# Performance work log

Measured on AMD Instinct MI355X. Metric: run time of the kernel, lower is better.

The kernel has to match this reference:

```python
import jax, jax.numpy as jnp
import numpy as np

N_NODES = 100000
N_EDGES = 1250000
IN_NDIM = 128
OUT_NDIM = 64


def setup_inputs() -> dict:
    key = jax.random.key(0)
    ks = jax.random.split(key, 8)
    return {
        "node_feats": jax.random.normal(ks[0], (N_NODES, IN_NDIM), dtype=jnp.float32),
        "edge_d": jax.random.uniform(ks[1], (N_EDGES, 1), dtype=jnp.float32),
        "W0": jax.random.normal(ks[2], (1, 1), dtype=jnp.float32),
        "W1": jax.random.normal(ks[3], (OUT_NDIM, IN_NDIM), dtype=jnp.float32) * (IN_NDIM ** -0.5),
        "W2": jax.random.normal(ks[4], (OUT_NDIM, IN_NDIM), dtype=jnp.float32) * (IN_NDIM ** -0.5),
        "Wa": jax.random.normal(ks[5], (1, 2 * OUT_NDIM + 1), dtype=jnp.float32) * (OUT_NDIM ** -0.5),
        "src": jax.random.randint(ks[6], (N_EDGES,), 0, N_NODES, dtype=jnp.int32),
        "dst": jax.random.randint(ks[7], (N_EDGES,), 0, N_NODES, dtype=jnp.int32),
    }


def reference(node_feats, edge_d, W0, W1, W2, Wa, src, dst):
    N = node_feats.shape[0]
    # fc1 / fc2 node projections (bias-free linears)
    z = node_feats @ W1.T            # [N, out_ndim]
    z_i = node_feats @ W2.T          # [N, out_ndim]
    # fc0 edge feature projection
    t = edge_d @ W0.T                # [E, 1]
    # gather per-edge endpoint features
    z_src = z[src]                   # [E, out_ndim]
    z_dst = z[dst]                   # [E, out_ndim]
    # attention logit: leaky_relu(attn_fc([z_src, z_dst, t]))
    a = jnp.concatenate([z_src, z_dst, t], axis=1) @ Wa.T   # [E, 1]
    e = jax.nn.leaky_relu(a[:, 0], 0.01)                      # torch default slope
    # segment softmax over incoming edges of each dst node
    m = jax.ops.segment_max(e, dst, num_segments=N)          # -inf for empty segs
    ex = jnp.exp(e - m[dst])
    denom = jax.ops.segment_sum(ex, dst, num_segments=N)
    alpha = ex / denom[dst]                                   # [E]
    # weighted scatter-sum of source messages
    z_neighbor = jax.ops.segment_sum(alpha[:, None] * z_src, dst, num_segments=N)
    h = jax.nn.relu(z_i + z_neighbor)
    return h
```

## Files before the change

kernel.cpp:

```cpp
#include <hip/hip_runtime.h>

#define N_NODES 100000
#define N_EDGES 1250000
#define IN_D 128
#define OUT_D 64
#define BSHIFT 8
#define NBUCK  391
#define CAP    4608
#define EPB    4096
#define NBLK_E 306
#define NBLK_G 1563

typedef __attribute__((ext_vector_type(8))) __bf16 bf16x8;
typedef __attribute__((ext_vector_type(4))) float floatx4;

__device__ __forceinline__ float2 up2(unsigned u) {
    return make_float2(__uint_as_float(u << 16),
                       __uint_as_float(u & 0xFFFF0000u));
}

__global__ __launch_bounds__(256) void fusedA_kernel(
    const float* __restrict__ x, const float* __restrict__ W1,
    const float* __restrict__ W2, const float* __restrict__ W0,
    const float* __restrict__ Wa,
    const int* __restrict__ dst, const int* __restrict__ src,
    const float* __restrict__ edge_d,
    int* __restrict__ gcur, uint2* __restrict__ payA,
    unsigned short* __restrict__ zb, unsigned short* __restrict__ zib,
    float* __restrict__ s1, float* __restrict__ s2)
{
    __shared__ __bf16 sB[16384];
    __shared__ float  sWa[128];
    __shared__ int    h[NBUCK];
    __shared__ int    lcur[NBUCK];

    const int t = threadIdx.x;

    if (blockIdx.x < NBLK_E) {
        const float tc = W0[0] * Wa[2 * OUT_D];
        for (int i = t; i < NBUCK; i += 256) h[i] = 0;
        __syncthreads();
        const int base = blockIdx.x * EPB;
        for (int k0 = 0; k0 < EPB; k0 += 1024) {
            int i = base + k0 + t * 4;
            if (i < N_EDGES) {
                int4 d4 = *(const int4*)(dst + i);
                atomicAdd(&h[d4.x >> BSHIFT], 1);
                atomicAdd(&h[d4.y >> BSHIFT], 1);
                atomicAdd(&h[d4.z >> BSHIFT], 1);
                atomicAdd(&h[d4.w >> BSHIFT], 1);
            }
        }
        __syncthreads();
        for (int b = t; b < NBUCK; b += 256) {
            int hc = h[b];
            int p = hc ? atomicAdd(&gcur[b], hc) : 0;
            lcur[b] = b * CAP + p;
        }
        __syncthreads();
        #define EMIT(dv, sv, ev)                                              \
            { int bk = (dv) >> BSHIFT;                                        \
              int pos = atomicAdd(&lcur[bk], 1);                              \
              if (pos < (bk + 1) * CAP)                                       \
                  payA[pos] = make_uint2((unsigned)(sv) |                     \
                                         ((unsigned)((dv) & 255) << 17),      \
                                         __float_as_uint(tc * (ev))); }
        for (int k0 = 0; k0 < EPB; k0 += 1024) {
            int i = base + k0 + t * 4;
            if (i < N_EDGES) {
                int4   d4 = *(const int4*)(dst + i);
                int4   s4 = *(const int4*)(src + i);
                float4 e4 = *(const float4*)(edge_d + i);
                EMIT(d4.x, s4.x, e4.x);
                EMIT(d4.y, s4.y, e4.y);
                EMIT(d4.z, s4.z, e4.z);
                EMIT(d4.w, s4.w, e4.w);
            }
        }
        #undef EMIT
        return;
    }

    #pragma unroll
    for (int g = 0; g < 8; ++g) {
        int gi = t + g * 256;
        int n  = gi >> 4;
        int k8 = gi & 15;
        const float* wrow = (n < 64) ? (W1 + n * 128) : (W2 + (n - 64) * 128);
        float4 v0 = *(const float4*)(wrow + k8 * 8);
        float4 v1 = *(const float4*)(wrow + k8 * 8 + 4);
        int lane = ((k8 & 3) << 4) | (n & 15);
        int off  = (((n >> 4) * 4 + (k8 >> 2)) * 64 + lane) * 8;
        bf16x8 bb;
        bb[0] = (__bf16)v0.x; bb[1] = (__bf16)v0.y;
        bb[2] = (__bf16)v0.z; bb[3] = (__bf16)v0.w;
        bb[4] = (__bf16)v1.x; bb[5] = (__bf16)v1.y;
        bb[6] = (__bf16)v1.z; bb[7] = (__bf16)v1.w;
        *(bf16x8*)(sB + off) = bb;
    }
    if (t < 128) sWa[t] = Wa[t];
    __syncthreads();

    const int lane = t & 63;
    const int wave = t >> 6;
    const int tile = (blockIdx.x - NBLK_E) * 4 + wave;
    if (tile * 16 >= N_NODES) return;

    const int n0 = tile * 16;
    const int m  = lane & 15;
    const int kb = lane >> 4;

    floatx4 acc[8];
    #pragma unroll
    for (int q = 0; q < 8; ++q) acc[q] = (floatx4)(0.f);

    const float* xrow = x + (size_t)(n0 + m) * IN_D;

    #pragma unroll
    for (int kc = 0; kc < 4; ++kc) {
        float4 v0 = *(const float4*)(xrow + kc * 32 + kb * 8);
        float4 v1 = *(const float4*)(xrow + kc * 32 + kb * 8 + 4);
        float xs[8] = {v0.x, v0.y, v0.z, v0.w, v1.x, v1.y, v1.z, v1.w};
        bf16x8 ahi, alo;
        #pragma unroll
        for (int j = 0; j < 8; ++j) {
            __bf16 hh = (__bf16)xs[j];
            ahi[j] = hh;
            alo[j] = (__bf16)(xs[j] - (float)hh);
        }
        #pragma unroll
        for (int nt = 0; nt < 8; ++nt) {
            int off = ((nt * 4 + kc) * 64 + lane) * 8;
            bf16x8 b = *(const bf16x8*)(sB + off);
            acc[nt] = __builtin_amdgcn_mfma_f32_16x16x32_bf16(ahi, b, acc[nt], 0, 0, 0);
            acc[nt] = __builtin_amdgcn_mfma_f32_16x16x32_bf16(alo, b, acc[nt], 0, 0, 0);
        }
    }

    #pragma unroll
    for (int nt = 0; nt < 8; ++nt) {
        int col = (nt & 3) * 16 + m;
        unsigned short* dp = (nt < 4) ? zb : zib;
        #pragma unroll
        for (int reg = 0; reg < 4; ++reg) {
            int row = n0 + kb * 4 + reg;
            __bf16 hh = (__bf16)acc[nt][reg];
            dp[(size_t)row * OUT_D + col] = *(unsigned short*)&hh;
        }
    }

    #pragma unroll
    for (int reg = 0; reg < 4; ++reg) {
        float p1 = 0.f, p2 = 0.f;
        #pragma unroll
        for (int nt = 0; nt < 4; ++nt) {
            float zv = acc[nt][reg];
            p1 += zv * sWa[nt * 16 + m];
            p2 += zv * sWa[64 + nt * 16 + m];
        }
        #pragma unroll
        for (int off = 8; off > 0; off >>= 1) {
            p1 += __shfl_xor(p1, off);
            p2 += __shfl_xor(p2, off);
        }
        if (m == 0) {
            int row = n0 + kb * 4 + reg;
            s1[row] = p1;
            s2[row] = p2;
        }
    }
}

__global__ __launch_bounds__(512) void passB_kernel(
    const int* __restrict__ gcur, const uint2* __restrict__ payA,
    int2* __restrict__ node_meta, uint2* __restrict__ payB)
{
    __shared__ int h[256];
    __shared__ int lc[256];
    __shared__ int sm[256];

    const int b = blockIdx.x, t = threadIdx.x;
    const int base = b * CAP;
    const int cnt = min(gcur[b], CAP);
    const int n0 = b << BSHIFT;

    if (t < 256) h[t] = 0;
    __syncthreads();

    for (int i0 = t * 4; i0 < cnt; i0 += 2048) {
        uint4 u0 = *(const uint4*)(payA + base + i0);
        uint4 u1 = *(const uint4*)(payA + base + i0 + 2);
        atomicAdd(&h[(u0.x >> 17) & 255], 1);
        if (i0 + 1 < cnt) atomicAdd(&h[(u0.z >> 17) & 255], 1);
        if (i0 + 2 < cnt) atomicAdd(&h[(u1.x >> 17) & 255], 1);
        if (i0 + 3 < cnt) atomicAdd(&h[(u1.z >> 17) & 255], 1);
    }
    __syncthreads();

    if (t < 256) {
        int v = h[t];
        sm[t] = v;
        __syncthreads();
        for (int off = 1; off < 256; off <<= 1) {
            int add = (t >= off) ? sm[t - off] : 0;
            __syncthreads();
            sm[t] += add;
            __syncthreads();
        }
        int start = base + sm[t] - v;
        lc[t] = start;
        if (n0 + t < N_NODES) node_meta[n0 + t] = make_int2(start, v);
    } else {
        __syncthreads();
        for (int off = 1; off < 256; off <<= 1) {
            __syncthreads(); __syncthreads();
        }
    }
    __syncthreads();

    #define PUT(xx, yy, ok)                                                   \
        if (ok) { int j = ((xx) >> 17) & 255;                                 \
                  int pos = atomicAdd(&lc[j], 1);                             \
                  payB[pos] = make_uint2((xx) & 0x1FFFFu, (yy)); }
    for (int i0 = t * 4; i0 < cnt; i0 += 2048) {
        uint4 u0 = *(const uint4*)(payA + base + i0);
        uint4 u1 = *(const uint4*)(payA + base + i0 + 2);
        PUT(u0.x, u0.y, true);
        PUT(u0.z, u0.w, i0 + 1 < cnt);
        PUT(u1.x, u1.y, i0 + 2 < cnt);
        PUT(u1.z, u1.w, i0 + 3 < cnt);
    }
    #undef PUT
}

__global__ __launch_bounds__(256) void gather_finalize_kernel(
    const int2* __restrict__ node_meta, const uint2* __restrict__ payB,
    const float* __restrict__ s1, const float* __restrict__ s2,
    const unsigned short* __restrict__ zb, const unsigned short* __restrict__ zib,
    float* __restrict__ out)
{
    __shared__ uint2 buf[8][32];

    const int lane = threadIdx.x & 63;
    const int wave = threadIdx.x >> 6;
    const int half = lane >> 5;
    const int lh   = lane & 31;
    const int nodeSlot = wave * 2 + half;
    const int d = blockIdx.x * 8 + nodeSlot;

    const int2 meta = node_meta[d];
    const int beg = meta.x;
    const int len = meta.y;
    const float s2d = s2[d];

    const int eC = lh >> 3;
    const int c  = lh & 7;

    float den = 0.f;
    float2 a0 = make_float2(0.f, 0.f), a1 = a0, a2 = a0, a3 = a0;

    for (int o = 0; o < len; o += 32) {
        int rem = len - o;
        bool v = lh < rem;
        uint2 p = payB[beg + o + (v ? lh : 0)];
        float ex = 0.f;
        if (v) {
            float a = __uint_as_float(p.y) + s1[p.x] + s2d;
            float e = (a > 0.f) ? a : 0.01f * a;
            ex = __expf(e);
            buf[nodeSlot][lh] = make_uint2(p.x, __float_as_uint(ex));
        }
        den += ex;

        int cnt = min(32, rem);
        for (int g = 0; g * 4 < cnt; ++g) {
            int j = g * 4 + eC;
            uint2 pe = buf[nodeSlot][(j < cnt) ? j : 0];
            float exe = (j < cnt) ? __uint_as_float(pe.y) : 0.f;
            uint4 zv = *(const uint4*)(zb + (size_t)pe.x * OUT_D + c * 8);
            float2 w0 = up2(zv.x), w1 = up2(zv.y), w2 = up2(zv.z), w3 = up2(zv.w);
            a0.x = fmaf(exe, w0.x, a0.x); a0.y = fmaf(exe, w0.y, a0.y);
            a1.x = fmaf(exe, w1.x, a1.x); a1.y = fmaf(exe, w1.y, a1.y);
            a2.x = fmaf(exe, w2.x, a2.x); a2.y = fmaf(exe, w2.y, a2.y);
            a3.x = fmaf(exe, w3.x, a3.x); a3.y = fmaf(exe, w3.y, a3.y);
        }
    }

    #pragma unroll
    for (int off = 16; off > 0; off >>= 1) den += __shfl_xor(den, off);
    #pragma unroll
    for (int off = 8; off <= 16; off <<= 1) {
        a0.x += __shfl_xor(a0.x, off); a0.y += __shfl_xor(a0.y, off);
        a1.x += __shfl_xor(a1.x, off); a1.y += __shfl_xor(a1.y, off);
        a2.x += __shfl_xor(a2.x, off); a2.y += __shfl_xor(a2.y, off);
        a3.x += __shfl_xor(a3.x, off); a3.y += __shfl_xor(a3.y, off);
    }

    if (lh < 8) {
        float inv = (den > 0.f) ? 1.f / den : 0.f;
        uint4 zv = *(const uint4*)(zib + (size_t)d * OUT_D + lh * 8);
        float2 w0 = up2(zv.x), w1 = up2(zv.y), w2 = up2(zv.z), w3 = up2(zv.w);
        float4 o0, o1;
        o0.x = fmaxf(w0.x + a0.x * inv, 0.f);
        o0.y = fmaxf(w0.y + a0.y * inv, 0.f);
        o0.z = fmaxf(w1.x + a1.x * inv, 0.f);
        o0.w = fmaxf(w1.y + a1.y * inv, 0.f);
        o1.x = fmaxf(w2.x + a2.x * inv, 0.f);
        o1.y = fmaxf(w2.y + a2.y * inv, 0.f);
        o1.z = fmaxf(w3.x + a3.x * inv, 0.f);
        o1.w = fmaxf(w3.y + a3.y * inv, 0.f);
        *(float4*)(out + (size_t)d * OUT_D + lh * 8)     = o0;
        *(float4*)(out + (size_t)d * OUT_D + lh * 8 + 4) = o1;
    }
}

extern "C" void kernel_launch(void* const* d_in, const int* in_sizes, int n_in,
                              void* d_out, int out_size, void* d_ws, size_t ws_size,
                              hipStream_t stream) {
    const float* node_feats = (const float*)d_in[0];
    const float* edge_d     = (const float*)d_in[1];
    const float* W0         = (const float*)d_in[2];
    const float* W1         = (const float*)d_in[3];
    const float* W2         = (const float*)d_in[4];
    const float* Wa         = (const float*)d_in[5];
    const int*   src        = (const int*)d_in[6];
    const int*   dst        = (const int*)d_in[7];
    float* out = (float*)d_out;

    char* ws = (char*)d_ws;
    uint2* payA = (uint2*)ws;    ws += (size_t)NBUCK * CAP * 8;
    uint2* payB = (uint2*)ws;    ws += (size_t)NBUCK * CAP * 8;
    unsigned short* zbuf = (unsigned short*)ws; ws += (size_t)N_NODES * OUT_D * 2;
    unsigned short* zib  = (unsigned short*)ws; ws += (size_t)N_NODES * OUT_D * 2;
    float* s1 = (float*)ws;      ws += (size_t)N_NODES * 4;
    float* s2 = (float*)ws;      ws += (size_t)N_NODES * 4;
    int2*  node_meta = (int2*)ws; ws += (size_t)N_NODES * 8;
    int*   gcur = (int*)ws;      ws += ((NBUCK + 3) & ~3) * 4;

    hipMemsetAsync(gcur, 0, NBUCK * 4, stream);

    fusedA_kernel<<<NBLK_E + NBLK_G, 256, 0, stream>>>(
        node_feats, W1, W2, W0, Wa, dst, src, edge_d,
        gcur, payA, zbuf, zib, s1, s2);

    passB_kernel<<<NBUCK, 512, 0, stream>>>(gcur, payA, node_meta, payB);

    gather_finalize_kernel<<<N_NODES / 8, 256, 0, stream>>>(
        node_meta, payB, s1, s2, zbuf, zib, out);
}
```

Before: 190.1 us.

## Replace second-level sort and gather with per-bucket LDS atomic accumulation

Buckets shrink to 128 destination nodes. The passB counting sort and the per-node gather kernel are replaced by a single kernel that streams each bucket's payload once. Each edge's exp weight and weighted source row are accumulated into a shared-memory numerator/denominator table with LDS float atomics, followed by an in-block finalize. This removes the payB write/read round trip, the node_meta array and one kernel launch. The cost is 65 shared atomics per edge, possible bank and address contention on hot destination rows, and uncoalesced per-thread 128-byte row loads from zb.

New measurement: 685.2 us. 260% more time.

```diff
diff --git a/kernel.cpp b/kernel.cpp
--- a/kernel.cpp
+++ b/kernel.cpp
@@ -4,9 +4,9 @@
 #define N_EDGES 1250000
 #define IN_D 128
 #define OUT_D 64
-#define BSHIFT 8
-#define NBUCK  391
-#define CAP    4608
+#define BSHIFT 7
+#define NBUCK  782
+#define CAP    2560
 #define EPB    4096
 #define NBLK_E 306
 #define NBLK_G 1563
@@ -63,7 +63,7 @@
               int pos = atomicAdd(&lcur[bk], 1);                              \
               if (pos < (bk + 1) * CAP)                                       \
                   payA[pos] = make_uint2((unsigned)(sv) |                     \
-                                         ((unsigned)((dv) & 255) << 17),      \
+                                         ((unsigned)((dv) & 127) << 17),      \
                                          __float_as_uint(tc * (ev))); }
         for (int k0 = 0; k0 < EPB; k0 += 1024) {
             int i = base + k0 + t * 4;
@@ -171,146 +171,84 @@
     }
 }
 
-__global__ __launch_bounds__(512) void passB_kernel(
+__global__ __launch_bounds__(512) void accum_finalize_kernel(
     const int* __restrict__ gcur, const uint2* __restrict__ payA,
-    int2* __restrict__ node_meta, uint2* __restrict__ payB)
-{
-    __shared__ int h[256];
-    __shared__ int lc[256];
-    __shared__ int sm[256];
-
-    const int b = blockIdx.x, t = threadIdx.x;
-    const int base = b * CAP;
-    const int cnt = min(gcur[b], CAP);
-    const int n0 = b << BSHIFT;
-
-    if (t < 256) h[t] = 0;
-    __syncthreads();
-
-    for (int i0 = t * 4; i0 < cnt; i0 += 2048) {
-        uint4 u0 = *(const uint4*)(payA + base + i0);
-        uint4 u1 = *(const uint4*)(payA + base + i0 + 2);
-        atomicAdd(&h[(u0.x >> 17) & 255], 1);
-        if (i0 + 1 < cnt) atomicAdd(&h[(u0.z >> 17) & 255], 1);
-        if (i0 + 2 < cnt) atomicAdd(&h[(u1.x >> 17) & 255], 1);
-        if (i0 + 3 < cnt) atomicAdd(&h[(u1.z >> 17) & 255], 1);
-    }
-    __syncthreads();
-
-    if (t < 256) {
-        int v = h[t];
-        sm[t] = v;
-        __syncthreads();
-        for (int off = 1; off < 256; off <<= 1) {
-            int add = (t >= off) ? sm[t - off] : 0;
-            __syncthreads();
-            sm[t] += add;
-            __syncthreads();
-        }
-        int start = base + sm[t] - v;
-        lc[t] = start;
-        if (n0 + t < N_NODES) node_meta[n0 + t] = make_int2(start, v);
-    } else {
-        __syncthreads();
-        for (int off = 1; off < 256; off <<= 1) {
-            __syncthreads(); __syncthreads();
-        }
-    }
-    __syncthreads();
-
-    #define PUT(xx, yy, ok)                                                   \
-        if (ok) { int j = ((xx) >> 17) & 255;                                 \
-                  int pos = atomicAdd(&lc[j], 1);                             \
-                  payB[pos] = make_uint2((xx) & 0x1FFFFu, (yy)); }
-    for (int i0 = t * 4; i0 < cnt; i0 += 2048) {
-        uint4 u0 = *(const uint4*)(payA + base + i0);
-        uint4 u1 = *(const uint4*)(payA + base + i0 + 2);
-        PUT(u0.x, u0.y, true);
-        PUT(u0.z, u0.w, i0 + 1 < cnt);
-        PUT(u1.x, u1.y, i0 + 2 < cnt);
-        PUT(u1.z, u1.w, i0 + 3 < cnt);
-    }
-    #undef PUT
-}
-
-__global__ __launch_bounds__(256) void gather_finalize_kernel(
-    const int2* __restrict__ node_meta, const uint2* __restrict__ payB,
     const float* __restrict__ s1, const float* __restrict__ s2,
     const unsigned short* __restrict__ zb, const unsigned short* __restrict__ zib,
     float* __restrict__ out)
 {
-    __shared__ uint2 buf[8][32];
-
-    const int lane = threadIdx.x & 63;
-    const int wave = threadIdx.x >> 6;
-    const int half = lane >> 5;
-    const int lh   = lane & 31;
-    const int nodeSlot = wave * 2 + half;
-    const int d = blockIdx.x * 8 + nodeSlot;
-
-    const int2 meta = node_meta[d];
-    const int beg = meta.x;
-    const int len = meta.y;
-    const float s2d = s2[d];
-
-    const int eC = lh >> 3;
-    const int c  = lh & 7;
-
-    float den = 0.f;
-    float2 a0 = make_float2(0.f, 0.f), a1 = a0, a2 = a0, a3 = a0;
-
-    for (int o = 0; o < len; o += 32) {
-        int rem = len - o;
-        bool v = lh < rem;
-        uint2 p = payB[beg + o + (v ? lh : 0)];
-        float ex = 0.f;
-        if (v) {
-            float a = __uint_as_float(p.y) + s1[p.x] + s2d;
-            float e = (a > 0.f) ? a : 0.01f * a;
-            ex = __expf(e);
-            buf[nodeSlot][lh] = make_uint2(p.x, __float_as_uint(ex));
-        }
-        den += ex;
-
-        int cnt = min(32, rem);
-        for (int g = 0; g * 4 < cnt; ++g) {
-            int j = g * 4 + eC;
-            uint2 pe = buf[nodeSlot][(j < cnt) ? j : 0];
-            float exe = (j < cnt) ? __uint_as_float(pe.y) : 0.f;
-            uint4 zv = *(const uint4*)(zb + (size_t)pe.x * OUT_D + c * 8);
-            float2 w0 = up2(zv.x), w1 = up2(zv.y), w2 = up2(zv.z), w3 = up2(zv.w);
-            a0.x = fmaf(exe, w0.x, a0.x); a0.y = fmaf(exe, w0.y, a0.y);
-            a1.x = fmaf(exe, w1.x, a1.x); a1.y = fmaf(exe, w1.y, a1.y);
-            a2.x = fmaf(exe, w2.x, a2.x); a2.y = fmaf(exe, w2.y, a2.y);
-            a3.x = fmaf(exe, w3.x, a3.x); a3.y = fmaf(exe, w3.y, a3.y);
-        }
-    }
-
-    #pragma unroll
-    for (int off = 16; off > 0; off >>= 1) den += __shfl_xor(den, off);
-    #pragma unroll
-    for (int off = 8; off <= 16; off <<= 1) {
-        a0.x += __shfl_xor(a0.x, off); a0.y += __shfl_xor(a0.y, off);
-        a1.x += __shfl_xor(a1.x, off); a1.y += __shfl_xor(a1.y, off);
-        a2.x += __shfl_xor(a2.x, off); a2.y += __shfl_xor(a2.y, off);
-        a3.x += __shfl_xor(a3.x, off); a3.y += __shfl_xor(a3.y, off);
-    }
-
-    if (lh < 8) {
-        float inv = (den > 0.f) ? 1.f / den : 0.f;
-        uint4 zv = *(const uint4*)(zib + (size_t)d * OUT_D + lh * 8);
-        float2 w0 = up2(zv.x), w1 = up2(zv.y), w2 = up2(zv.z), w3 = up2(zv.w);
-        float4 o0, o1;
-        o0.x = fmaxf(w0.x + a0.x * inv, 0.f);
-        o0.y = fmaxf(w0.y + a0.y * inv, 0.f);
-        o0.z = fmaxf(w1.x + a1.x * inv, 0.f);
-        o0.w = fmaxf(w1.y + a1.y * inv, 0.f);
-        o1.x = fmaxf(w2.x + a2.x * inv, 0.f);
-        o1.y = fmaxf(w2.y + a2.y * inv, 0.f);
-        o1.z = fmaxf(w3.x + a3.x * inv, 0.f);
-        o1.w = fmaxf(w3.y + a3.y * inv, 0.f);
-        *(float4*)(out + (size_t)d * OUT_D + lh * 8)     = o0;
-        *(float4*)(out + (size_t)d * OUT_D + lh * 8 + 4) = o1;
+    __shared__ float num[128][65];
+    __shared__ float den[128];
+    __shared__ float s2s[128];
+
+    const int b = blockIdx.x, t = threadIdx.x;
+    const int n0 = b << BSHIFT;
+
+    for (int i = t; i < 128 * 65; i += 512) (&num[0][0])[i] = 0.f;
+    if (t < 128) {
+        den[t] = 0.f;
+        int node = n0 + t;
+        s2s[t] = (node < N_NODES) ? s2[node] : 0.f;
+    }
+    __syncthreads();
+
+    const int base = b * CAP;
+    const int cnt = min(gcur[b], CAP);
+
+    for (int i0 = 0; i0 < cnt; i0 += 512) {
+        int i = i0 + t;
+        if (i < cnt) {
+            uint2 p = payA[base + i];
+            int srcn = p.x & 0x1FFFF;
+            int dl   = (p.x >> 17) & 127;
+            float a  = __uint_as_float(p.y) + s1[srcn] + s2s[dl];
+            float e  = (a > 0.f) ? a : 0.01f * a;
+            float ex = __expf(e);
+            float* nrow = num[dl];
+            atomicAdd(&den[dl], ex);
+            const uint4* zp = (const uint4*)(zb + (size_t)srcn * OUT_D);
+            uint4 q0 = zp[0], q1 = zp[1], q2 = zp[2], q3 = zp[3];
+            #define ACC2(w, k) { float2 f = up2(w);                 \
+                atomicAdd(nrow + (k),     ex * f.x);                \
+                atomicAdd(nrow + (k) + 1, ex * f.y); }
+            ACC2(q0.x,  0) ACC2(q0.y,  2) ACC2(q0.z,  4) ACC2(q0.w,  6)
+            ACC2(q1.x,  8) ACC2(q1.y, 10) ACC2(q1.z, 12) ACC2(q1.w, 14)
+            ACC2(q2.x, 16) ACC2(q2.y, 18) ACC2(q2.z, 20) ACC2(q2.w, 22)
+            ACC2(q3.x, 24) ACC2(q3.y, 26) ACC2(q3.z, 28) ACC2(q3.w, 30)
+            uint4 q4 = zp[4], q5 = zp[5], q6 = zp[6], q7 = zp[7];
+            ACC2(q4.x, 32) ACC2(q4.y, 34) ACC2(q4.z, 36) ACC2(q4.w, 38)
+            ACC2(q5.x, 40) ACC2(q5.y, 42) ACC2(q5.z, 44) ACC2(q5.w, 46)
+            ACC2(q6.x, 48) ACC2(q6.y, 50) ACC2(q6.z, 52) ACC2(q6.w, 54)
+            ACC2(q7.x, 56) ACC2(q7.y, 58) ACC2(q7.z, 60) ACC2(q7.w, 62)
+            #undef ACC2
+        }
+    }
+    __syncthreads();
+
+    const int n = t >> 2;
+    const int node = n0 + n;
+    if (node < N_NODES) {
+        const int dq = (t & 3) * 16;
+        float dn = den[n];
+        float inv = (dn > 0.f) ? 1.f / dn : 0.f;
+        const float* nr = &num[n][dq];
+        const unsigned short* zr = zib + (size_t)node * OUT_D + dq;
+        uint4 z0 = *(const uint4*)zr;
+        uint4 z1 = *(const uint4*)(zr + 8);
+        float* op = out + (size_t)node * OUT_D + dq;
+        float2 f; float4 o;
+        f = up2(z0.x); o.x = fmaxf(f.x + nr[ 0]*inv, 0.f); o.y = fmaxf(f.y + nr[ 1]*inv, 0.f);
+        f = up2(z0.y); o.z = fmaxf(f.x + nr[ 2]*inv, 0.f); o.w = fmaxf(f.y + nr[ 3]*inv, 0.f);
+        ((float4*)op)[0] = o;
+        f = up2(z0.z); o.x = fmaxf(f.x + nr[ 4]*inv, 0.f); o.y = fmaxf(f.y + nr[ 5]*inv, 0.f);
+        f = up2(z0.w); o.z = fmaxf(f.x + nr[ 6]*inv, 0.f); o.w = fmaxf(f.y + nr[ 7]*inv, 0.f);
+        ((float4*)op)[1] = o;
+        f = up2(z1.x); o.x = fmaxf(f.x + nr[ 8]*inv, 0.f); o.y = fmaxf(f.y + nr[ 9]*inv, 0.f);
+        f = up2(z1.y); o.z = fmaxf(f.x + nr[10]*inv, 0.f); o.w = fmaxf(f.y + nr[11]*inv, 0.f);
+        ((float4*)op)[2] = o;
+        f = up2(z1.z); o.x = fmaxf(f.x + nr[12]*inv, 0.f); o.y = fmaxf(f.y + nr[13]*inv, 0.f);
+        f = up2(z1.w); o.z = fmaxf(f.x + nr[14]*inv, 0.f); o.w = fmaxf(f.y + nr[15]*inv, 0.f);
+        ((float4*)op)[3] = o;
     }
 }
 
@@ -329,12 +267,10 @@
 
     char* ws = (char*)d_ws;
     uint2* payA = (uint2*)ws;    ws += (size_t)NBUCK * CAP * 8;
-    uint2* payB = (uint2*)ws;    ws += (size_t)NBUCK * CAP * 8;
     unsigned short* zbuf = (unsigned short*)ws; ws += (size_t)N_NODES * OUT_D * 2;
     unsigned short* zib  = (unsigned short*)ws; ws += (size_t)N_NODES * OUT_D * 2;
     float* s1 = (float*)ws;      ws += (size_t)N_NODES * 4;
     float* s2 = (float*)ws;      ws += (size_t)N_NODES * 4;
-    int2*  node_meta = (int2*)ws; ws += (size_t)N_NODES * 8;
     int*   gcur = (int*)ws;      ws += ((NBUCK + 3) & ~3) * 4;
 
     hipMemsetAsync(gcur, 0, NBUCK * 4, stream);
@@ -343,8 +279,6 @@
         node_feats, W1, W2, W0, Wa, dst, src, edge_d,
         gcur, payA, zbuf, zib, s1, s2);
 
-    passB_kernel<<<NBUCK, 512, 0, stream>>>(gcur, payA, node_meta, payB);
-
-    gather_finalize_kernel<<<N_NODES / 8, 256, 0, stream>>>(
-        node_meta, payB, s1, s2, zbuf, zib, out);
-}
+    accum_finalize_kernel<<<NBUCK, 512, 0, stream>>>(
+        gcur, payA, s1, s2, zbuf, zib, out);
+}
```

## Fuse per-bucket local sort into gather kernel using shared-memory sorted edges

Applied to the files above, without the earlier changes.

Merges the second-pass bucket sort and the gather/finalize kernel into one kernel per bucket: each block histograms, prefix-scans and scatters its bucket's edges into shared memory, then processes its 128 nodes directly from that sorted buffer. The bucket width halves so the sorted bucket fits in LDS (2560 entries), removing the payB global write/read, the node_meta array and one kernel launch. In exchange there are only 782 blocks of 512 threads with large LDS usage, so occupancy and load balance for the memory-latency-bound gather may drop, and the tighter bucket capacity raises overflow risk for skewed degree distributions.

Measured after the change: 185.8 us. 1.02x faster.

```diff
diff --git a/kernel.cpp b/kernel.cpp
--- a/kernel.cpp
+++ b/kernel.cpp
@@ -4,9 +4,9 @@
 #define N_EDGES 1250000
 #define IN_D 128
 #define OUT_D 64
-#define BSHIFT 8
-#define NBUCK  391
-#define CAP    4608
+#define BSHIFT 7
+#define NBUCK  782
+#define CAP    2560
 #define EPB    4096
 #define NBLK_E 306
 #define NBLK_G 1563
@@ -63,7 +63,7 @@
               int pos = atomicAdd(&lcur[bk], 1);                              \
               if (pos < (bk + 1) * CAP)                                       \
                   payA[pos] = make_uint2((unsigned)(sv) |                     \
-                                         ((unsigned)((dv) & 255) << 17),      \
+                                         ((unsigned)((dv) & 127) << 17),      \
                                          __float_as_uint(tc * (ev))); }
         for (int k0 = 0; k0 < EPB; k0 += 1024) {
             int i = base + k0 + t * 4;
@@ -171,146 +171,128 @@
     }
 }
 
-__global__ __launch_bounds__(512) void passB_kernel(
+__global__ __launch_bounds__(512) void sortgather_kernel(
     const int* __restrict__ gcur, const uint2* __restrict__ payA,
-    int2* __restrict__ node_meta, uint2* __restrict__ payB)
-{
-    __shared__ int h[256];
-    __shared__ int lc[256];
-    __shared__ int sm[256];
-
-    const int b = blockIdx.x, t = threadIdx.x;
-    const int base = b * CAP;
-    const int cnt = min(gcur[b], CAP);
-    const int n0 = b << BSHIFT;
-
-    if (t < 256) h[t] = 0;
-    __syncthreads();
-
-    for (int i0 = t * 4; i0 < cnt; i0 += 2048) {
-        uint4 u0 = *(const uint4*)(payA + base + i0);
-        uint4 u1 = *(const uint4*)(payA + base + i0 + 2);
-        atomicAdd(&h[(u0.x >> 17) & 255], 1);
-        if (i0 + 1 < cnt) atomicAdd(&h[(u0.z >> 17) & 255], 1);
-        if (i0 + 2 < cnt) atomicAdd(&h[(u1.x >> 17) & 255], 1);
-        if (i0 + 3 < cnt) atomicAdd(&h[(u1.z >> 17) & 255], 1);
-    }
-    __syncthreads();
-
-    if (t < 256) {
-        int v = h[t];
-        sm[t] = v;
-        __syncthreads();
-        for (int off = 1; off < 256; off <<= 1) {
-            int add = (t >= off) ? sm[t - off] : 0;
-            __syncthreads();
-            sm[t] += add;
-            __syncthreads();
-        }
-        int start = base + sm[t] - v;
-        lc[t] = start;
-        if (n0 + t < N_NODES) node_meta[n0 + t] = make_int2(start, v);
-    } else {
-        __syncthreads();
-        for (int off = 1; off < 256; off <<= 1) {
-            __syncthreads(); __syncthreads();
-        }
-    }
-    __syncthreads();
-
-    #define PUT(xx, yy, ok)                                                   \
-        if (ok) { int j = ((xx) >> 17) & 255;                                 \
-                  int pos = atomicAdd(&lc[j], 1);                             \
-                  payB[pos] = make_uint2((xx) & 0x1FFFFu, (yy)); }
-    for (int i0 = t * 4; i0 < cnt; i0 += 2048) {
-        uint4 u0 = *(const uint4*)(payA + base + i0);
-        uint4 u1 = *(const uint4*)(payA + base + i0 + 2);
-        PUT(u0.x, u0.y, true);
-        PUT(u0.z, u0.w, i0 + 1 < cnt);
-        PUT(u1.x, u1.y, i0 + 2 < cnt);
-        PUT(u1.z, u1.w, i0 + 3 < cnt);
-    }
-    #undef PUT
-}
-
-__global__ __launch_bounds__(256) void gather_finalize_kernel(
-    const int2* __restrict__ node_meta, const uint2* __restrict__ payB,
     const float* __restrict__ s1, const float* __restrict__ s2,
     const unsigned short* __restrict__ zb, const unsigned short* __restrict__ zib,
     float* __restrict__ out)
 {
-    __shared__ uint2 buf[8][32];
-
-    const int lane = threadIdx.x & 63;
-    const int wave = threadIdx.x >> 6;
+    __shared__ uint2 sorted[CAP];
+    __shared__ int   h[128];
+    __shared__ int   st[128];
+    __shared__ int   lc[128];
+    __shared__ float s2s[128];
+    __shared__ uint2 buf[16][32];
+
+    const int b = blockIdx.x, t = threadIdx.x;
+    const int n0 = b << BSHIFT;
+    const int base = b * CAP;
+    const int cnt = min(gcur[b], CAP);
+
+    if (t < 128) {
+        h[t] = 0;
+        int node = n0 + t;
+        s2s[t] = (node < N_NODES) ? s2[node] : 0.f;
+    }
+    __syncthreads();
+
+    for (int i = t; i < cnt; i += 512) {
+        uint2 p = payA[base + i];
+        atomicAdd(&h[(p.x >> 17) & 127], 1);
+    }
+    __syncthreads();
+
+    int v = 0;
+    if (t < 128) { v = h[t]; st[t] = v; }
+    for (int off = 1; off < 128; off <<= 1) {
+        __syncthreads();
+        int add = (t < 128 && t >= off) ? st[t - off] : 0;
+        __syncthreads();
+        if (t < 128) st[t] += add;
+    }
+    __syncthreads();
+    if (t < 128) { int s = st[t] - v; st[t] = s; lc[t] = s; }
+    __syncthreads();
+
+    for (int i = t; i < cnt; i += 512) {
+        uint2 p = payA[base + i];
+        int dl = (p.x >> 17) & 127;
+        int pos = atomicAdd(&lc[dl], 1);
+        sorted[pos] = make_uint2(p.x & 0x1FFFFu, p.y);
+    }
+    __syncthreads();
+
+    const int lane = t & 63;
+    const int wave = t >> 6;
     const int half = lane >> 5;
     const int lh   = lane & 31;
-    const int nodeSlot = wave * 2 + half;
-    const int d = blockIdx.x * 8 + nodeSlot;
-
-    const int2 meta = node_meta[d];
-    const int beg = meta.x;
-    const int len = meta.y;
-    const float s2d = s2[d];
-
+    const int slot = wave * 2 + half;
     const int eC = lh >> 3;
     const int c  = lh & 7;
 
-    float den = 0.f;
-    float2 a0 = make_float2(0.f, 0.f), a1 = a0, a2 = a0, a3 = a0;
-
-    for (int o = 0; o < len; o += 32) {
-        int rem = len - o;
-        bool v = lh < rem;
-        uint2 p = payB[beg + o + (v ? lh : 0)];
-        float ex = 0.f;
-        if (v) {
-            float a = __uint_as_float(p.y) + s1[p.x] + s2d;
-            float e = (a > 0.f) ? a : 0.01f * a;
-            ex = __expf(e);
-            buf[nodeSlot][lh] = make_uint2(p.x, __float_as_uint(ex));
-        }
-        den += ex;
-
-        int cnt = min(32, rem);
-        for (int g = 0; g * 4 < cnt; ++g) {
-            int j = g * 4 + eC;
-            uint2 pe = buf[nodeSlot][(j < cnt) ? j : 0];
-            float exe = (j < cnt) ? __uint_as_float(pe.y) : 0.f;
-            uint4 zv = *(const uint4*)(zb + (size_t)pe.x * OUT_D + c * 8);
+    for (int r = 0; r < 8; ++r) {
+        const int ln   = slot + r * 16;
+        const int node = n0 + ln;
+        const int beg  = st[ln];
+        const int len  = h[ln];
+        const float s2d = s2s[ln];
+
+        float den = 0.f;
+        float2 a0 = make_float2(0.f, 0.f), a1 = a0, a2 = a0, a3 = a0;
+
+        for (int o = 0; o < len; o += 32) {
+            int rem = len - o;
+            bool vv = lh < rem;
+            uint2 p = sorted[beg + o + (vv ? lh : 0)];
+            float ex = 0.f;
+            if (vv) {
+                float a = __uint_as_float(p.y) + s1[p.x] + s2d;
+                float e = (a > 0.f) ? a : 0.01f * a;
+                ex = __expf(e);
+                buf[slot][lh] = make_uint2(p.x, __float_as_uint(ex));
+            }
+            den += ex;
+
+            int cnt2 = min(32, rem);
+            for (int g = 0; g * 4 < cnt2; ++g) {
+                int j = g * 4 + eC;
+                uint2 pe = buf[slot][(j < cnt2) ? j : 0];
+                float exe = (j < cnt2) ? __uint_as_float(pe.y) : 0.f;
+                uint4 zv = *(const uint4*)(zb + (size_t)pe.x * OUT_D + c * 8);
+                float2 w0 = up2(zv.x), w1 = up2(zv.y), w2 = up2(zv.z), w3 = up2(zv.w);
+                a0.x = fmaf(exe, w0.x, a0.x); a0.y = fmaf(exe, w0.y, a0.y);
+                a1.x = fmaf(exe, w1.x, a1.x); a1.y = fmaf(exe, w1.y, a1.y);
+                a2.x = fmaf(exe, w2.x, a2.x); a2.y = fmaf(exe, w2.y, a2.y);
+                a3.x = fmaf(exe, w3.x, a3.x); a3.y = fmaf(exe, w3.y, a3.y);
+            }
+        }
+
+        #pragma unroll
+        for (int off = 16; off > 0; off >>= 1) den += __shfl_xor(den, off);
+        #pragma unroll
+        for (int off = 8; off <= 16; off <<= 1) {
+            a0.x += __shfl_xor(a0.x, off); a0.y += __shfl_xor(a0.y, off);
+            a1.x += __shfl_xor(a1.x, off); a1.y += __shfl_xor(a1.y, off);
+            a2.x += __shfl_xor(a2.x, off); a2.y += __shfl_xor(a2.y, off);
+            a3.x += __shfl_xor(a3.x, off); a3.y += __shfl_xor(a3.y, off);
+        }
+
+        if (lh < 8 && node < N_NODES) {
+            float inv = (den > 0.f) ? 1.f / den : 0.f;
+            uint4 zv = *(const uint4*)(zib + (size_t)node * OUT_D + lh * 8);
             float2 w0 = up2(zv.x), w1 = up2(zv.y), w2 = up2(zv.z), w3 = up2(zv.w);
-            a0.x = fmaf(exe, w0.x, a0.x); a0.y = fmaf(exe, w0.y, a0.y);
-            a1.x = fmaf(exe, w1.x, a1.x); a1.y = fmaf(exe, w1.y, a1.y);
-            a2.x = fmaf(exe, w2.x, a2.x); a2.y = fmaf(exe, w2.y, a2.y);
-            a3.x = fmaf(exe, w3.x, a3.x); a3.y = fmaf(exe, w3.y, a3.y);
-        }
-    }
-
-    #pragma unroll
-    for (int off = 16; off > 0; off >>= 1) den += __shfl_xor(den, off);
-    #pragma unroll
-    for (int off = 8; off <= 16; off <<= 1) {
-        a0.x += __shfl_xor(a0.x, off); a0.y += __shfl_xor(a0.y, off);
-        a1.x += __shfl_xor(a1.x, off); a1.y += __shfl_xor(a1.y, off);
-        a2.x += __shfl_xor(a2.x, off); a2.y += __shfl_xor(a2.y, off);
-        a3.x += __shfl_xor(a3.x, off); a3.y += __shfl_xor(a3.y, off);
-    }
-
-    if (lh < 8) {
-        float inv = (den > 0.f) ? 1.f / den : 0.f;
-        uint4 zv = *(const uint4*)(zib + (size_t)d * OUT_D + lh * 8);
-        float2 w0 = up2(zv.x), w1 = up2(zv.y), w2 = up2(zv.z), w3 = up2(zv.w);
-        float4 o0, o1;
-        o0.x = fmaxf(w0.x + a0.x * inv, 0.f);
-        o0.y = fmaxf(w0.y + a0.y * inv, 0.f);
-        o0.z = fmaxf(w1.x + a1.x * inv, 0.f);
-        o0.w = fmaxf(w1.y + a1.y * inv, 0.f);
-        o1.x = fmaxf(w2.x + a2.x * inv, 0.f);
-        o1.y = fmaxf(w2.y + a2.y * inv, 0.f);
-        o1.z = fmaxf(w3.x + a3.x * inv, 0.f);
-        o1.w = fmaxf(w3.y + a3.y * inv, 0.f);
-        *(float4*)(out + (size_t)d * OUT_D + lh * 8)     = o0;
-        *(float4*)(out + (size_t)d * OUT_D + lh * 8 + 4) = o1;
+            float4 o0, o1;
+            o0.x = fmaxf(w0.x + a0.x * inv, 0.f);
+            o0.y = fmaxf(w0.y + a0.y * inv, 0.f);
+            o0.z = fmaxf(w1.x + a1.x * inv, 0.f);
+            o0.w = fmaxf(w1.y + a1.y * inv, 0.f);
+            o1.x = fmaxf(w2.x + a2.x * inv, 0.f);
+            o1.y = fmaxf(w2.y + a2.y * inv, 0.f);
+            o1.z = fmaxf(w3.x + a3.x * inv, 0.f);
+            o1.w = fmaxf(w3.y + a3.y * inv, 0.f);
+            *(float4*)(out + (size_t)node * OUT_D + lh * 8)     = o0;
+            *(float4*)(out + (size_t)node * OUT_D + lh * 8 + 4) = o1;
+        }
     }
 }
 
@@ -329,12 +311,10 @@
 
     char* ws = (char*)d_ws;
     uint2* payA = (uint2*)ws;    ws += (size_t)NBUCK * CAP * 8;
-    uint2* payB = (uint2*)ws;    ws += (size_t)NBUCK * CAP * 8;
     unsigned short* zbuf = (unsigned short*)ws; ws += (size_t)N_NODES * OUT_D * 2;
     unsigned short* zib  = (unsigned short*)ws; ws += (size_t)N_NODES * OUT_D * 2;
     float* s1 = (float*)ws;      ws += (size_t)N_NODES * 4;
     float* s2 = (float*)ws;      ws += (size_t)N_NODES * 4;
-    int2*  node_meta = (int2*)ws; ws += (size_t)N_NODES * 8;
     int*   gcur = (int*)ws;      ws += ((NBUCK + 3) & ~3) * 4;
 
     hipMemsetAsync(gcur, 0, NBUCK * 4, stream);
@@ -343,8 +323,6 @@
         node_feats, W1, W2, W0, Wa, dst, src, edge_d,
         gcur, payA, zbuf, zib, s1, s2);
 
-    passB_kernel<<<NBUCK, 512, 0, stream>>>(gcur, payA, node_meta, payB);
-
-    gather_finalize_kernel<<<N_NODES / 8, 256, 0, stream>>>(
-        node_meta, payB, s1, s2, zbuf, zib, out);
+    sortgather_kernel<<<NBUCK, 512, 0, stream>>>(
+        gcur, payA, s1, s2, zbuf, zib, out);
 }
```
